# Kernel optimization log

Hardware: AMD Instinct MI355X
Metric: run time of the kernel (lower is better)

The kernel has to match this reference:

```python
import jax, jax.numpy as jnp
import numpy as np

N_GRAPHS = 100
BN_EPS = 1e-5
L = 4


def batch_norm(x, gamma, beta):
    # torch BatchNorm1d in training mode: biased batch statistics over the node dim
    mu = jnp.mean(x, axis=0)
    var = jnp.var(x, axis=0)
    return gamma * (x - mu) * jax.lax.rsqrt(var + BN_EPS) + beta


def setup_inputs() -> dict:
    key = jax.random.key(0)
    ks = jax.random.split(key, 24)
    N, E, IN, H, C = 50000, 600000, 128, 128, 10
    s = 0.05
    inp = {
        "h": jax.random.normal(ks[0], (N, IN), jnp.float32),
        "snorm_n": jax.random.uniform(ks[1], (N, 1), jnp.float32),
        "edge_src": jax.random.randint(ks[2], (E,), 0, N, jnp.int32),
        "edge_dst": jax.random.randint(ks[3], (E,), 0, N, jnp.int32),
        "graph_ids": jnp.sort(jax.random.randint(ks[4], (N,), 0, N_GRAPHS, jnp.int32)),
        # embedding_h
        "emb_W": jax.random.normal(ks[5], (IN, H), jnp.float32) * s,
        "emb_b": jnp.zeros((H,), jnp.float32),
        # per-layer GIN params, stacked over L layers
        "eps": jnp.zeros((L,), jnp.float32),
        "W1": jax.random.normal(ks[6], (L, H, H), jnp.float32) * s,
        "b1": jnp.zeros((L, H), jnp.float32),
        "g1": jnp.ones((L, H), jnp.float32),   # MLP internal BN gamma
        "be1": jnp.zeros((L, H), jnp.float32),  # MLP internal BN beta
        "W2": jax.random.normal(ks[7], (L, H, H), jnp.float32) * s,
        "b2": jnp.zeros((L, H), jnp.float32),
        "ga": jnp.ones((L, H), jnp.float32),    # ApplyNodeFunc BN gamma
        "ba": jnp.zeros((L, H), jnp.float32),
        "gl": jnp.ones((L, H), jnp.float32),    # GINLayer node BN gamma
        "bl": jnp.zeros((L, H), jnp.float32),
        # linears_prediction (L+1 of them)
        "pred_W": jax.random.normal(ks[8], (L + 1, H, C), jnp.float32) * s,
        "pred_b": jnp.zeros((L + 1, C), jnp.float32),
    }
    return inp


def reference(h, snorm_n, edge_src, edge_dst, graph_ids, emb_W, emb_b, eps,
              W1, b1, g1, be1, W2, b2, ga, ba, gl, bl, pred_W, pred_b):
    N = h.shape[0]
    h = h @ emb_W + emb_b  # embedding_h
    hidden_rep = [h]
    for i in range(L):
        h_in = h
        # sum-aggregate neighbor features (irregular gather + scatter-add)
        neigh = jax.ops.segment_sum(h[edge_src], edge_dst, num_segments=N)
        z = (1.0 + eps[i]) * h + neigh
        # ApplyNodeFunc: MLP (lin->BN->relu->lin) then BN then relu
        z = jax.nn.relu(batch_norm(z @ W1[i] + b1[i], g1[i], be1[i]))
        z = z @ W2[i] + b2[i]
        z = jax.nn.relu(batch_norm(z, ga[i], ba[i]))
        z = z * snorm_n                      # graph_norm
        z = batch_norm(z, gl[i], bl[i])      # batch_norm
        z = jax.nn.relu(z)
        h = h_in + z                         # residual (dropout p=0)
        hidden_rep.append(h)
    score = jnp.zeros((N_GRAPHS, pred_W.shape[-1]), h.dtype)
    for i, hr in enumerate(hidden_rep):
        pooled = jax.ops.segment_sum(hr, graph_ids, num_segments=N_GRAPHS)
        score = score + pooled @ pred_W[i] + pred_b[i]
    return score
```

## Files before the change

### kernel.cpp

```cpp
#include <hip/hip_runtime.h>

#define HD __device__ __forceinline__

static constexpr int H = 128;
static constexpr int G = 100;
static constexpr int L = 4;
static constexpr int C = 10;
static constexpr int DEGCAP = 64;
static constexpr int CNT_PAD = 50048;

typedef __attribute__((ext_vector_type(8))) short short8;
typedef __attribute__((ext_vector_type(4))) float f32x4;

HD float bf2f(unsigned int u16) {
    return __uint_as_float(u16 << 16);
}
HD unsigned int f2bf(float f) {
    unsigned int u = __float_as_uint(f);
    u += 0x7fffu + ((u >> 16) & 1u);
    return u >> 16;
}

__global__ __launch_bounds__(256) void prep_kernel(
    const float* __restrict__ embW, const float* __restrict__ W1, const float* __restrict__ W2,
    unsigned short* __restrict__ WT, unsigned short* __restrict__ Hb,
    const int* __restrict__ src, const int* __restrict__ dst, int E,
    int* __restrict__ cnt, int* __restrict__ esrc) {
    int b = blockIdx.x;
    if (b < 576) {
        int mat = b >> 6;
        int bx = b & 63;
        if (b == 0 && threadIdx.x < 64)
            ((unsigned int*)Hb)[threadIdx.x] = 0u;
        const float* s = (mat == 0) ? embW
                       : (mat <= L) ? W1 + (size_t)(mat - 1) * H * H
                                    : W2 + (size_t)(mat - 1 - L) * H * H;
        int t = bx * 256 + threadIdx.x;
        int col = t >> 7, k = t & 127;
        WT[(size_t)mat * H * H + col * H + k] = (unsigned short)f2bf(s[(size_t)k * H + col]);
    } else {
        int e = (b - 576) * 256 + threadIdx.x;
        if (e < E) {
            int d = dst[e];
            int pos = atomicAdd(&cnt[d], 1) & (DEGCAP - 1);
            esrc[(size_t)d * DEGCAP + pos] = src[e] + 1;
        }
    }
}

__global__ __launch_bounds__(1024, 2) void aggemm_kernel(
    const unsigned short* __restrict__ HbZ, const int* __restrict__ cnt,
    const int* __restrict__ esrc, const float* __restrict__ eps, int layer,
    const unsigned short* __restrict__ WT, const float* __restrict__ bias,
    unsigned short* __restrict__ outB, int N,
    float* __restrict__ sum_out, float* __restrict__ sq_out,
    int* __restrict__ ctr, int ntiles) {
    __shared__ unsigned short As[64 * 136];
    __shared__ int epsh[64][16];
    __shared__ int degsh[64];
    __shared__ int tilesh;
    int tid = threadIdx.x;
    int w = tid >> 6, lane = tid & 63, q = lane >> 4, m = lane & 15;
    float e1 = 1.0f + eps[layer];

    int mrow = (w >> 2) * 16;
    int colbase = (w & 3) * 32;
    short8 bfrag[2][4];
#pragma unroll
    for (int nt = 0; nt < 2; ++nt) {
        const unsigned short* wc = WT + (size_t)(colbase + nt * 16 + m) * H;
#pragma unroll
        for (int kk = 0; kk < 4; ++kk)
            bfrag[nt][kk] = *(const short8*)&wc[kk * 32 + q * 8];
    }
    float bs2[2] = {bias[colbase + m], bias[colbase + 16 + m]};

    for (;;) {
        if (tid == 0) tilesh = atomicAdd(ctr, 1);
        __syncthreads();
        int tile = tilesh;
        if (tile >= ntiles) break;
        int row0 = tile * 64;

        {
            int n = tid >> 4, u = tid & 15;
            int nd = min(row0 + n, N - 1);
            epsh[n][u] = esrc[(size_t)nd * DEGCAP + u];
            if (tid < 64) {
                int nn = row0 + tid;
                degsh[tid] = (nn < N) ? min(cnt[nn], DEGCAP) : 0;
            }
        }
        __syncthreads();

        {
            const unsigned int* H2 = (const unsigned int*)HbZ;
#pragma unroll
            for (int i = 0; i < 4; ++i) {
                int r = w * 4 + i;
                int node = row0 + r;
                unsigned int out = 0;
                if (node < N) {
                    unsigned int hv = H2[(size_t)(node + 1) * 64 + lane];
                    float ax = e1 * bf2f(hv & 0xffffu);
                    float ay = e1 * bf2f(hv >> 16);
                    int deg = degsh[r];
                    if (deg > 0) {
                        unsigned int v[16];
#pragma unroll
                        for (int u = 0; u < 16; ++u) v[u] = H2[(size_t)epsh[r][u] * 64 + lane];
                        float sx[4] = {0.f, 0.f, 0.f, 0.f}, sy[4] = {0.f, 0.f, 0.f, 0.f};
#pragma unroll
                        for (int u = 0; u < 16; ++u) {
                            sx[u & 3] += bf2f(v[u] & 0xffffu);
                            sy[u & 3] += bf2f(v[u] >> 16);
                        }
                        ax += (sx[0] + sx[1]) + (sx[2] + sx[3]);
                        ay += (sy[0] + sy[1]) + (sy[2] + sy[3]);
                        if (deg > 16) {
                            const int* ep = esrc + (size_t)node * DEGCAP;
                            int degPad = min((deg + 15) & ~15, DEGCAP);
                            for (int j = 16; j < degPad; j += 16) {
                                unsigned int vv[16];
#pragma unroll
                                for (int u = 0; u < 16; ++u) vv[u] = H2[(size_t)ep[j + u] * 64 + lane];
                                float tx[4] = {0.f, 0.f, 0.f, 0.f}, ty[4] = {0.f, 0.f, 0.f, 0.f};
#pragma unroll
                                for (int u = 0; u < 16; ++u) {
                                    tx[u & 3] += bf2f(vv[u] & 0xffffu);
                                    ty[u & 3] += bf2f(vv[u] >> 16);
                                }
                                ax += (tx[0] + tx[1]) + (tx[2] + tx[3]);
                                ay += (ty[0] + ty[1]) + (ty[2] + ty[3]);
                            }
                        }
                    }
                    out = f2bf(ax) | (f2bf(ay) << 16);
                }
                *(unsigned int*)&As[r * 136 + lane * 2] = out;
            }
        }
        __syncthreads();

        f32x4 acc[2] = {(f32x4){0.f, 0.f, 0.f, 0.f}, (f32x4){0.f, 0.f, 0.f, 0.f}};
#pragma unroll
        for (int kk = 0; kk < 4; ++kk) {
            short8 af = *(const short8*)&As[(mrow + m) * 136 + kk * 32 + q * 8];
#pragma unroll
            for (int nt = 0; nt < 2; ++nt)
                acc[nt] = __builtin_amdgcn_mfma_f32_16x16x32_bf16(af, bfrag[nt][kk], acc[nt], 0, 0, 0);
        }

        float s[2] = {0.f, 0.f}, qq[2] = {0.f, 0.f};
#pragma unroll
        for (int nt = 0; nt < 2; ++nt) {
            int gcol = colbase + nt * 16 + m;
#pragma unroll
            for (int rg = 0; rg < 4; ++rg) {
                int grow = row0 + mrow + q * 4 + rg;
                float v = acc[nt][rg] + bs2[nt];
                if (grow < N) {
                    outB[(size_t)grow * H + gcol] = (unsigned short)f2bf(v);
                    s[nt] += v;
                    qq[nt] += v * v;
                }
            }
        }
#pragma unroll
        for (int nt = 0; nt < 2; ++nt) {
            s[nt] += __shfl_xor(s[nt], 16); s[nt] += __shfl_xor(s[nt], 32);
            qq[nt] += __shfl_xor(qq[nt], 16); qq[nt] += __shfl_xor(qq[nt], 32);
        }
        __syncthreads();
        float* SS = (float*)As;
        float* QQ = SS + 4 * H;
        if (q == 0) {
#pragma unroll
            for (int nt = 0; nt < 2; ++nt) {
                int col = colbase + nt * 16 + m;
                SS[(w >> 2) * H + col] = s[nt];
                QQ[(w >> 2) * H + col] = qq[nt];
            }
        }
        __syncthreads();
        if (tid < H) {
            atomicAdd(&sum_out[tid], SS[tid] + SS[H + tid] + SS[2 * H + tid] + SS[3 * H + tid]);
            atomicAdd(&sq_out[tid], QQ[tid] + QQ[H + tid] + QQ[2 * H + tid] + QQ[3 * H + tid]);
        }
    }
}

template <bool ABF16, bool TRANS, bool STATS, bool POOLF, bool HOFF>
__global__ __launch_bounds__(256, 4) void mgemm_kernel(
    const float* __restrict__ Af, const unsigned short* __restrict__ Ab,
    const unsigned short* __restrict__ WT, const float* __restrict__ bias,
    const float* __restrict__ sum_in, const float* __restrict__ sq_in,
    const float* __restrict__ gam, const float* __restrict__ bet, float invN,
    unsigned short* __restrict__ outB,
    int N, float* __restrict__ sum_out, float* __restrict__ sq_out,
    const int* __restrict__ gids, float* __restrict__ pool) {
    __shared__ unsigned short As[64 * 136];
    __shared__ float cas[H], ccs[H];
    int tid = threadIdx.x;
    int w = tid >> 6, lane = tid & 63, q = lane >> 4, m = lane & 15;
    int row0 = blockIdx.x * 64;
    int colbase = w * 32;

    short8 bfrag[2][4];
#pragma unroll
    for (int nt = 0; nt < 2; ++nt) {
        const unsigned short* wc = WT + (size_t)(colbase + nt * 16 + m) * H;
#pragma unroll
        for (int kk = 0; kk < 4; ++kk)
            bfrag[nt][kk] = *(const short8*)&wc[kk * 32 + q * 8];
    }

    if (TRANS) {
        if (tid < H) {
            float mu = sum_in[tid] * invN;
            float var = sq_in[tid] * invN - mu * mu;
            float inv = rsqrtf(var + 1e-5f);
            float a = gam[tid] * inv;
            cas[tid] = a;
            ccs[tid] = bet[tid] - mu * a;
        }
        __syncthreads();
    }

    {
        int cc = tid & 15, rg = tid >> 4;
        int c0 = cc * 8;
        float a8[8], b8[8];
        if (TRANS) {
#pragma unroll
            for (int j = 0; j < 8; ++j) { a8[j] = cas[c0 + j]; b8[j] = ccs[c0 + j]; }
        }
#pragma unroll
        for (int rr = 0; rr < 4; ++rr) {
            int r = rg * 4 + rr;
            int gr = row0 + r;
            uint4 o = {0u, 0u, 0u, 0u};
            if (ABF16 && !TRANS) {
                if (gr < N) o = *(const uint4*)&Ab[(size_t)gr * H + c0];
            } else {
                float v[8] = {0.f, 0.f, 0.f, 0.f, 0.f, 0.f, 0.f, 0.f};
                if (gr < N) {
                    if (ABF16) {
                        uint4 x = *(const uint4*)&Ab[(size_t)gr * H + c0];
                        v[0] = bf2f(x.x & 0xffffu); v[1] = bf2f(x.x >> 16);
                        v[2] = bf2f(x.y & 0xffffu); v[3] = bf2f(x.y >> 16);
                        v[4] = bf2f(x.z & 0xffffu); v[5] = bf2f(x.z >> 16);
                        v[6] = bf2f(x.w & 0xffffu); v[7] = bf2f(x.w >> 16);
                    } else {
                        float4 x0 = *(const float4*)&Af[(size_t)gr * H + c0];
                        float4 x1 = *(const float4*)&Af[(size_t)gr * H + c0 + 4];
                        v[0] = x0.x; v[1] = x0.y; v[2] = x0.z; v[3] = x0.w;
                        v[4] = x1.x; v[5] = x1.y; v[6] = x1.z; v[7] = x1.w;
                    }
                }
                if (TRANS) {
#pragma unroll
                    for (int j = 0; j < 8; ++j) v[j] = fmaxf(a8[j] * v[j] + b8[j], 0.f);
                }
                o.x = f2bf(v[0]) | (f2bf(v[1]) << 16);
                o.y = f2bf(v[2]) | (f2bf(v[3]) << 16);
                o.z = f2bf(v[4]) | (f2bf(v[5]) << 16);
                o.w = f2bf(v[6]) | (f2bf(v[7]) << 16);
            }
            *(uint4*)&As[r * 136 + c0] = o;
        }
    }
    __syncthreads();

    f32x4 acc[4][2];
#pragma unroll
    for (int mt = 0; mt < 4; ++mt)
#pragma unroll
        for (int nt = 0; nt < 2; ++nt) acc[mt][nt] = (f32x4){0.f, 0.f, 0.f, 0.f};
#pragma unroll
    for (int kk = 0; kk < 4; ++kk) {
        short8 af[4];
#pragma unroll
        for (int mt = 0; mt < 4; ++mt)
            af[mt] = *(const short8*)&As[(mt * 16 + m) * 136 + kk * 32 + q * 8];
#pragma unroll
        for (int mt = 0; mt < 4; ++mt)
#pragma unroll
            for (int nt = 0; nt < 2; ++nt)
                acc[mt][nt] = __builtin_amdgcn_mfma_f32_16x16x32_bf16(
                    af[mt], bfrag[nt][kk], acc[mt][nt], 0, 0, 0);
    }

    float bs2[2] = {bias[colbase + m], bias[colbase + 16 + m]};
    float s[2] = {0.f, 0.f}, qq[2] = {0.f, 0.f};
#pragma unroll
    for (int mt = 0; mt < 4; ++mt)
#pragma unroll
        for (int nt = 0; nt < 2; ++nt) {
            int gcol = colbase + nt * 16 + m;
#pragma unroll
            for (int rg = 0; rg < 4; ++rg) {
                int grow = row0 + mt * 16 + q * 4 + rg;
                float v = acc[mt][nt][rg] + bs2[nt];
                if (grow < N) {
                    outB[(size_t)(HOFF ? grow + 1 : grow) * H + gcol] = (unsigned short)f2bf(v);
                    if (STATS) {
                        s[nt] += v;
                        qq[nt] += v * v;
                    }
                }
            }
        }

    if (STATS) {
#pragma unroll
        for (int nt = 0; nt < 2; ++nt) {
            float sv = s[nt], qv = qq[nt];
            sv += __shfl_xor(sv, 16); sv += __shfl_xor(sv, 32);
            qv += __shfl_xor(qv, 16); qv += __shfl_xor(qv, 32);
            if (q == 0) {
                atomicAdd(&sum_out[colbase + nt * 16 + m], sv);
                atomicAdd(&sq_out[colbase + nt * 16 + m], qv);
            }
        }
    }

    if (POOLF) {
        int g0 = gids[row0];
        int gL = gids[min(row0 + 63, N - 1)];
        float s0[2] = {0.f, 0.f}, s1[2] = {0.f, 0.f};
#pragma unroll
        for (int mt = 0; mt < 4; ++mt)
#pragma unroll
            for (int rg = 0; rg < 4; ++rg) {
                int grow = row0 + mt * 16 + q * 4 + rg;
                if (grow < N) {
                    int g = gids[grow];
#pragma unroll
                    for (int nt = 0; nt < 2; ++nt) {
                        float v = acc[mt][nt][rg] + bs2[nt];
                        if (g == g0) s0[nt] += v;
                        else if (g == gL) s1[nt] += v;
                        else atomicAdd(&pool[g * H + colbase + nt * 16 + m], v);
                    }
                }
            }
#pragma unroll
        for (int nt = 0; nt < 2; ++nt) {
            int col = colbase + nt * 16 + m;
            float sv = s0[nt];
            sv += __shfl_xor(sv, 16); sv += __shfl_xor(sv, 32);
            if (q == 0) atomicAdd(&pool[g0 * H + col], sv);
            if (gL != g0) {
                float tv = s1[nt];
                tv += __shfl_xor(tv, 16); tv += __shfl_xor(tv, 32);
                if (q == 0) atomicAdd(&pool[gL * H + col], tv);
            }
        }
    }
}

__global__ __launch_bounds__(256) void statsv_kernel(const unsigned short* __restrict__ UB,
                                                     const float* __restrict__ snorm,
                                                     const float* __restrict__ sum2, const float* __restrict__ sq2,
                                                     const float* __restrict__ ga, const float* __restrict__ ba,
                                                     float invN, int N,
                                                     float* __restrict__ sum3, float* __restrict__ sq3) {
    __shared__ float cas[H], ccs[H];
    int t = threadIdx.x;
    if (t < H) {
        float m = sum2[t] * invN;
        float var = sq2[t] * invN - m * m;
        float inv = rsqrtf(var + 1e-5f);
        float a = ga[t] * inv;
        cas[t] = a;
        ccs[t] = ba[t] - m * a;
    }
    __syncthreads();
    int col2 = t & 63, part = t >> 6;
    int c0 = col2 * 2, c1 = c0 + 1;
    float a0 = cas[c0], b0 = ccs[c0], a1 = cas[c1], b1 = ccs[c1];
    float s0 = 0.f, q0 = 0.f, s1 = 0.f, q1 = 0.f;
    const unsigned int* U2 = (const unsigned int*)UB;
    for (int r0 = blockIdx.x * 16 + part * 4; r0 < N; r0 += gridDim.x * 16) {
        unsigned int vv[4];
        float sn4[4];
#pragma unroll
        for (int k = 0; k < 4; ++k) {
            int r = r0 + k;
            bool ok = r < N;
            sn4[k] = ok ? snorm[r] : 0.f;
            vv[k] = ok ? U2[(size_t)r * 64 + col2] : 0u;
        }
#pragma unroll
        for (int k = 0; k < 4; ++k) {
            float v0 = fmaxf(a0 * bf2f(vv[k] & 0xffffu) + b0, 0.f) * sn4[k];
            float v1 = fmaxf(a1 * bf2f(vv[k] >> 16) + b1, 0.f) * sn4[k];
            s0 += v0; q0 += v0 * v0;
            s1 += v1; q1 += v1 * v1;
        }
    }
    __shared__ float S[4][H], Q[4][H];
    S[part][c0] = s0; S[part][c1] = s1;
    Q[part][c0] = q0; Q[part][c1] = q1;
    __syncthreads();
    if (t < H) {
        atomicAdd(&sum3[t], S[0][t] + S[1][t] + S[2][t] + S[3][t]);
        atomicAdd(&sq3[t], Q[0][t] + Q[1][t] + Q[2][t] + Q[3][t]);
    }
}

__global__ __launch_bounds__(256) void tail_kernel(unsigned short* __restrict__ HbZ,
                                                   const unsigned short* __restrict__ UB,
                                                   const float* __restrict__ snorm,
                                                   const float* __restrict__ sum2, const float* __restrict__ sq2,
                                                   const float* __restrict__ ga, const float* __restrict__ ba,
                                                   const float* __restrict__ sum3, const float* __restrict__ sq3,
                                                   const float* __restrict__ gl, const float* __restrict__ bl,
                                                   float invN, const int* __restrict__ gids,
                                                   float* __restrict__ pool, int N) {
    __shared__ float ca2[H], cc2[H], ca3[H], cc3[H];
    __shared__ float PS[16][H];
    int t = threadIdx.x;
    if (t < H) {
        float m2 = sum2[t] * invN, v2 = sq2[t] * invN - m2 * m2;
        float i2 = rsqrtf(v2 + 1e-5f), a2 = ga[t] * i2;
        ca2[t] = a2; cc2[t] = ba[t] - m2 * a2;
        float m3 = sum3[t] * invN, v3 = sq3[t] * invN - m3 * m3;
        float i3 = rsqrtf(v3 + 1e-5f), a3 = gl[t] * i3;
        ca3[t] = a3; cc3[t] = bl[t] - m3 * a3;
    }
    __syncthreads();
    int row0 = blockIdx.x * 32;
    int colg = t & 15, rowg = t >> 4;
    int c0 = colg * 8;
    float A2[8], B2[8], A3[8], B3[8];
#pragma unroll
    for (int j = 0; j < 8; ++j) {
        A2[j] = ca2[c0 + j]; B2[j] = cc2[c0 + j];
        A3[j] = ca3[c0 + j]; B3[j] = cc3[c0 + j];
    }
    int g0 = gids[row0];
    int gL = gids[min(row0 + 31, N - 1)];
    float p0[8] = {0.f, 0.f, 0.f, 0.f, 0.f, 0.f, 0.f, 0.f};
    float p1[8] = {0.f, 0.f, 0.f, 0.f, 0.f, 0.f, 0.f, 0.f};

    uint4 uv[2], hv[2];
    float sn2[2];
    int gg[2];
#pragma unroll
    for (int rr = 0; rr < 2; ++rr) {
        int grow = row0 + rowg * 2 + rr;
        bool ok = grow < N;
        sn2[rr] = ok ? snorm[grow] : 0.f;
        gg[rr] = ok ? gids[grow] : g0;
        uv[rr] = ok ? *(const uint4*)&UB[(size_t)grow * H + c0] : (uint4){0u, 0u, 0u, 0u};
        hv[rr] = ok ? *(const uint4*)&HbZ[(size_t)(grow + 1) * H + c0] : (uint4){0u, 0u, 0u, 0u};
    }
#pragma unroll
    for (int rr = 0; rr < 2; ++rr) {
        int grow = row0 + rowg * 2 + rr;
        if (grow < N) {
            float u[8] = {bf2f(uv[rr].x & 0xffffu), bf2f(uv[rr].x >> 16),
                          bf2f(uv[rr].y & 0xffffu), bf2f(uv[rr].y >> 16),
                          bf2f(uv[rr].z & 0xffffu), bf2f(uv[rr].z >> 16),
                          bf2f(uv[rr].w & 0xffffu), bf2f(uv[rr].w >> 16)};
            float h[8] = {bf2f(hv[rr].x & 0xffffu), bf2f(hv[rr].x >> 16),
                          bf2f(hv[rr].y & 0xffffu), bf2f(hv[rr].y >> 16),
                          bf2f(hv[rr].z & 0xffffu), bf2f(hv[rr].z >> 16),
                          bf2f(hv[rr].w & 0xffffu), bf2f(hv[rr].w >> 16)};
#pragma unroll
            for (int j = 0; j < 8; ++j) {
                float v = fmaxf(A2[j] * u[j] + B2[j], 0.f) * sn2[rr];
                h[j] += fmaxf(A3[j] * v + B3[j], 0.f);
            }
            uint4 hb;
            hb.x = f2bf(h[0]) | (f2bf(h[1]) << 16);
            hb.y = f2bf(h[2]) | (f2bf(h[3]) << 16);
            hb.z = f2bf(h[4]) | (f2bf(h[5]) << 16);
            hb.w = f2bf(h[6]) | (f2bf(h[7]) << 16);
            *(uint4*)&HbZ[(size_t)(grow + 1) * H + c0] = hb;
            int g = gg[rr];
            if (g == g0) {
#pragma unroll
                for (int j = 0; j < 8; ++j) p0[j] += h[j];
            } else if (g == gL) {
#pragma unroll
                for (int j = 0; j < 8; ++j) p1[j] += h[j];
            } else {
#pragma unroll
                for (int j = 0; j < 8; ++j) atomicAdd(&pool[g * H + c0 + j], h[j]);
            }
        }
    }
#pragma unroll
    for (int j = 0; j < 8; ++j) PS[rowg][c0 + j] = p0[j];
    __syncthreads();
    if (t < H) {
        float s = 0.f;
#pragma unroll
        for (int g = 0; g < 16; ++g) s += PS[g][t];
        atomicAdd(&pool[g0 * H + t], s);
    }
    if (gL != g0) {
        __syncthreads();
#pragma unroll
        for (int j = 0; j < 8; ++j) PS[rowg][c0 + j] = p1[j];
        __syncthreads();
        if (t < H) {
            float s = 0.f;
#pragma unroll
            for (int g = 0; g < 16; ++g) s += PS[g][t];
            atomicAdd(&pool[gL * H + t], s);
        }
    }
}

__global__ __launch_bounds__(128) void final_kernel(const float* __restrict__ pool,
                                                    const float* __restrict__ pw,
                                                    const float* __restrict__ pb,
                                                    float* __restrict__ out) {
    int g = blockIdx.x, t = threadIdx.x;
    float acc[C];
#pragma unroll
    for (int c = 0; c < C; ++c) acc[c] = 0.f;
#pragma unroll
    for (int i = 0; i <= L; ++i) {
        float p = pool[(size_t)(i * G + g) * H + t];
        const float* wrow = pw + (size_t)(i * H + t) * C;
#pragma unroll
        for (int c = 0; c < C; ++c) acc[c] += p * wrow[c];
    }
#pragma unroll
    for (int c = 0; c < C; ++c) {
        float v = acc[c];
        v += __shfl_xor(v, 1);  v += __shfl_xor(v, 2);  v += __shfl_xor(v, 4);
        v += __shfl_xor(v, 8);  v += __shfl_xor(v, 16); v += __shfl_xor(v, 32);
        acc[c] = v;
    }
    __shared__ float Ws[2][C];
    if ((t & 63) == 0) {
        int wv = t >> 6;
#pragma unroll
        for (int c = 0; c < C; ++c) Ws[wv][c] = acc[c];
    }
    __syncthreads();
    if (t < C) {
        float s = Ws[0][t] + Ws[1][t];
#pragma unroll
        for (int i = 0; i <= L; ++i) s += pb[i * C + t];
        out[g * C + t] = s;
    }
}

extern "C" void kernel_launch(void* const* d_in, const int* in_sizes, int n_in,
                              void* d_out, int out_size, void* d_ws, size_t ws_size,
                              hipStream_t stream) {
    const float* h_in  = (const float*)d_in[0];
    const float* snorm = (const float*)d_in[1];
    const int* esrc_in = (const int*)d_in[2];
    const int* edst_in = (const int*)d_in[3];
    const int* gids    = (const int*)d_in[4];
    const float* embW = (const float*)d_in[5];
    const float* embB = (const float*)d_in[6];
    const float* eps  = (const float*)d_in[7];
    const float* W1   = (const float*)d_in[8];
    const float* b1   = (const float*)d_in[9];
    const float* g1   = (const float*)d_in[10];
    const float* be1  = (const float*)d_in[11];
    const float* W2   = (const float*)d_in[12];
    const float* b2   = (const float*)d_in[13];
    const float* ga   = (const float*)d_in[14];
    const float* ba   = (const float*)d_in[15];
    const float* gl   = (const float*)d_in[16];
    const float* bl   = (const float*)d_in[17];
    const float* predW = (const float*)d_in[18];
    const float* predB = (const float*)d_in[19];

    const int N = in_sizes[0] / H;
    const int E = in_sizes[2];
    const float invN = 1.0f / (float)N;

    float* ws = (float*)d_ws;
    float* POOL = ws;
    float* STATS = POOL + (size_t)(L + 1) * G * H;
    int* CTR = (int*)(STATS + (size_t)L * 6 * H);
    int* CNT = CTR + 64;
    int* ESRC = CNT + CNT_PAD;
    unsigned short* WT = (unsigned short*)(ESRC + (size_t)N * DEGCAP);
    unsigned short* Hb = WT + (size_t)9 * H * H;
    unsigned short* ZB = Hb + (size_t)(N + 1) * H;
    unsigned short* TB = ZB + (size_t)N * H;
    unsigned short* UB = ZB;

    size_t zbytes = ((size_t)(L + 1) * G * H + (size_t)L * 6 * H + 64 + CNT_PAD + (size_t)N * DEGCAP) * 4;
    hipMemsetAsync(POOL, 0, zbytes, stream);

    int prep_blocks = 576 + (E + 255) / 256;
    prep_kernel<<<prep_blocks, 256, 0, stream>>>(embW, W1, W2, WT, Hb,
                                                 esrc_in, edst_in, E, CNT, ESRC);

    int gblocks = (N + 63) / 64;
    mgemm_kernel<false, false, false, true, true><<<gblocks, 256, 0, stream>>>(
        h_in, nullptr, WT, embB, nullptr, nullptr, nullptr, nullptr, invN,
        Hb, N, nullptr, nullptr, gids, POOL);

    for (int i = 0; i < L; ++i) {
        float* S1 = STATS + (size_t)i * 6 * H;
        float* Q1 = S1 + H;
        float* S2 = Q1 + H;
        float* Q2 = S2 + H;
        float* S3 = Q2 + H;
        float* Q3 = S3 + H;
        aggemm_kernel<<<512, 1024, 0, stream>>>(
            Hb, CNT, ESRC, eps, i, WT + (size_t)(1 + i) * H * H, b1 + (size_t)i * H,
            TB, N, S1, Q1, CTR + i, gblocks);
        mgemm_kernel<true, true, true, false, false><<<gblocks, 256, 0, stream>>>(
            nullptr, TB, WT + (size_t)(1 + L + i) * H * H, b2 + (size_t)i * H,
            S1, Q1, g1 + (size_t)i * H, be1 + (size_t)i * H, invN,
            UB, N, S2, Q2, nullptr, nullptr);
        statsv_kernel<<<1024, 256, 0, stream>>>(UB, snorm, S2, Q2,
                                                ga + (size_t)i * H, ba + (size_t)i * H, invN, N, S3, Q3);
        tail_kernel<<<(N + 31) / 32, 256, 0, stream>>>(Hb, UB, snorm,
                                                       S2, Q2, ga + (size_t)i * H, ba + (size_t)i * H,
                                                       S3, Q3, gl + (size_t)i * H, bl + (size_t)i * H,
                                                       invN, gids, POOL + (size_t)(i + 1) * G * H, N);
    }
    final_kernel<<<G, 128, 0, stream>>>(POOL, predW, predB, (float*)d_out);
}
```

Measured before the change: 608.4 us.

## Fuse second GEMM, BN stats and tail into one grid-barrier layer kernel

New measurement: 1.031 ms. +69.4%, slower.

```diff
diff --git a/kernel.cpp b/kernel.cpp
--- a/kernel.cpp
+++ b/kernel.cpp
@@ -19,6 +19,25 @@
     unsigned int u = __float_as_uint(f);
     u += 0x7fffu + ((u >> 16) & 1u);
     return u >> 16;
+}
+
+HD float aload(const float* p) {
+    return __hip_atomic_load(p, __ATOMIC_RELAXED, __HIP_MEMORY_SCOPE_AGENT);
+}
+
+HD void gridbar(int* arr, int* rel, int nblk, int tid) {
+    __syncthreads();
+    if (tid == 0) {
+        __threadfence();
+        int t = __hip_atomic_fetch_add(arr, 1, __ATOMIC_ACQ_REL, __HIP_MEMORY_SCOPE_AGENT);
+        if (t == nblk - 1) {
+            __hip_atomic_store(rel, 1, __ATOMIC_RELEASE, __HIP_MEMORY_SCOPE_AGENT);
+        } else {
+            while (__hip_atomic_load(rel, __ATOMIC_ACQUIRE, __HIP_MEMORY_SCOPE_AGENT) == 0)
+                __builtin_amdgcn_s_sleep(2);
+        }
+    }
+    __syncthreads();
 }
 
 __global__ __launch_bounds__(256) void prep_kernel(
@@ -190,17 +209,11 @@
     }
 }
 
-template <bool ABF16, bool TRANS, bool STATS, bool POOLF, bool HOFF>
-__global__ __launch_bounds__(256, 4) void mgemm_kernel(
-    const float* __restrict__ Af, const unsigned short* __restrict__ Ab,
-    const unsigned short* __restrict__ WT, const float* __restrict__ bias,
-    const float* __restrict__ sum_in, const float* __restrict__ sq_in,
-    const float* __restrict__ gam, const float* __restrict__ bet, float invN,
-    unsigned short* __restrict__ outB,
-    int N, float* __restrict__ sum_out, float* __restrict__ sq_out,
-    const int* __restrict__ gids, float* __restrict__ pool) {
+__global__ __launch_bounds__(256, 4) void embed_kernel(
+    const float* __restrict__ Af, const unsigned short* __restrict__ WT,
+    const float* __restrict__ bias, unsigned short* __restrict__ outB,
+    int N, const int* __restrict__ gids, float* __restrict__ pool) {
     __shared__ unsigned short As[64 * 136];
-    __shared__ float cas[H], ccs[H];
     int tid = threadIdx.x;
     int w = tid >> 6, lane = tid & 63, q = lane >> 4, m = lane & 15;
     int row0 = blockIdx.x * 64;
@@ -215,53 +228,149 @@
             bfrag[nt][kk] = *(const short8*)&wc[kk * 32 + q * 8];
     }
 
-    if (TRANS) {
-        if (tid < H) {
-            float mu = sum_in[tid] * invN;
-            float var = sq_in[tid] * invN - mu * mu;
-            float inv = rsqrtf(var + 1e-5f);
-            float a = gam[tid] * inv;
-            cas[tid] = a;
-            ccs[tid] = bet[tid] - mu * a;
-        }
-        __syncthreads();
-    }
-
     {
         int cc = tid & 15, rg = tid >> 4;
         int c0 = cc * 8;
-        float a8[8], b8[8];
-        if (TRANS) {
-#pragma unroll
-            for (int j = 0; j < 8; ++j) { a8[j] = cas[c0 + j]; b8[j] = ccs[c0 + j]; }
-        }
 #pragma unroll
         for (int rr = 0; rr < 4; ++rr) {
             int r = rg * 4 + rr;
             int gr = row0 + r;
             uint4 o = {0u, 0u, 0u, 0u};
-            if (ABF16 && !TRANS) {
-                if (gr < N) o = *(const uint4*)&Ab[(size_t)gr * H + c0];
-            } else {
-                float v[8] = {0.f, 0.f, 0.f, 0.f, 0.f, 0.f, 0.f, 0.f};
-                if (gr < N) {
-                    if (ABF16) {
-                        uint4 x = *(const uint4*)&Ab[(size_t)gr * H + c0];
-                        v[0] = bf2f(x.x & 0xffffu); v[1] = bf2f(x.x >> 16);
-                        v[2] = bf2f(x.y & 0xffffu); v[3] = bf2f(x.y >> 16);
-                        v[4] = bf2f(x.z & 0xffffu); v[5] = bf2f(x.z >> 16);
-                        v[6] = bf2f(x.w & 0xffffu); v[7] = bf2f(x.w >> 16);
-                    } else {
-                        float4 x0 = *(const float4*)&Af[(size_t)gr * H + c0];
-                        float4 x1 = *(const float4*)&Af[(size_t)gr * H + c0 + 4];
-                        v[0] = x0.x; v[1] = x0.y; v[2] = x0.z; v[3] = x0.w;
-                        v[4] = x1.x; v[5] = x1.y; v[6] = x1.z; v[7] = x1.w;
-                    }
+            if (gr < N) {
+                float4 x0 = *(const float4*)&Af[(size_t)gr * H + c0];
+                float4 x1 = *(const float4*)&Af[(size_t)gr * H + c0 + 4];
+                o.x = f2bf(x0.x) | (f2bf(x0.y) << 16);
+                o.y = f2bf(x0.z) | (f2bf(x0.w) << 16);
+                o.z = f2bf(x1.x) | (f2bf(x1.y) << 16);
+                o.w = f2bf(x1.z) | (f2bf(x1.w) << 16);
+            }
+            *(uint4*)&As[r * 136 + c0] = o;
+        }
+    }
+    __syncthreads();
+
+    f32x4 acc[4][2];
+#pragma unroll
+    for (int mt = 0; mt < 4; ++mt)
+#pragma unroll
+        for (int nt = 0; nt < 2; ++nt) acc[mt][nt] = (f32x4){0.f, 0.f, 0.f, 0.f};
+#pragma unroll
+    for (int kk = 0; kk < 4; ++kk) {
+        short8 af[4];
+#pragma unroll
+        for (int mt = 0; mt < 4; ++mt)
+            af[mt] = *(const short8*)&As[(mt * 16 + m) * 136 + kk * 32 + q * 8];
+#pragma unroll
+        for (int mt = 0; mt < 4; ++mt)
+#pragma unroll
+            for (int nt = 0; nt < 2; ++nt)
+                acc[mt][nt] = __builtin_amdgcn_mfma_f32_16x16x32_bf16(
+                    af[mt], bfrag[nt][kk], acc[mt][nt], 0, 0, 0);
+    }
+
+    float bs2[2] = {bias[colbase + m], bias[colbase + 16 + m]};
+#pragma unroll
+    for (int mt = 0; mt < 4; ++mt)
+#pragma unroll
+        for (int nt = 0; nt < 2; ++nt) {
+            int gcol = colbase + nt * 16 + m;
+#pragma unroll
+            for (int rg = 0; rg < 4; ++rg) {
+                int grow = row0 + mt * 16 + q * 4 + rg;
+                float v = acc[mt][nt][rg] + bs2[nt];
+                if (grow < N) outB[(size_t)(grow + 1) * H + gcol] = (unsigned short)f2bf(v);
+            }
+        }
+
+    int g0 = gids[row0];
+    int gL = gids[min(row0 + 63, N - 1)];
+    float s0[2] = {0.f, 0.f}, s1[2] = {0.f, 0.f};
+#pragma unroll
+    for (int mt = 0; mt < 4; ++mt)
+#pragma unroll
+        for (int rg = 0; rg < 4; ++rg) {
+            int grow = row0 + mt * 16 + q * 4 + rg;
+            if (grow < N) {
+                int g = gids[grow];
+#pragma unroll
+                for (int nt = 0; nt < 2; ++nt) {
+                    float v = acc[mt][nt][rg] + bs2[nt];
+                    if (g == g0) s0[nt] += v;
+                    else if (g == gL) s1[nt] += v;
+                    else atomicAdd(&pool[g * H + colbase + nt * 16 + m], v);
                 }
-                if (TRANS) {
-#pragma unroll
-                    for (int j = 0; j < 8; ++j) v[j] = fmaxf(a8[j] * v[j] + b8[j], 0.f);
-                }
+            }
+        }
+#pragma unroll
+    for (int nt = 0; nt < 2; ++nt) {
+        int col = colbase + nt * 16 + m;
+        float sv = s0[nt];
+        sv += __shfl_xor(sv, 16); sv += __shfl_xor(sv, 32);
+        if (q == 0) atomicAdd(&pool[g0 * H + col], sv);
+        if (gL != g0) {
+            float tv = s1[nt];
+            tv += __shfl_xor(tv, 16); tv += __shfl_xor(tv, 32);
+            if (q == 0) atomicAdd(&pool[gL * H + col], tv);
+        }
+    }
+}
+
+__global__ __launch_bounds__(256, 4) void layer_kernel(
+    const unsigned short* __restrict__ TB, const unsigned short* __restrict__ WT2,
+    const float* __restrict__ b2v,
+    const float* __restrict__ S1, const float* __restrict__ Q1,
+    const float* __restrict__ g1v, const float* __restrict__ be1v,
+    const float* __restrict__ snorm,
+    float* __restrict__ S2, float* __restrict__ Q2,
+    float* __restrict__ S3, float* __restrict__ Q3,
+    const float* __restrict__ gav, const float* __restrict__ bav,
+    const float* __restrict__ glv, const float* __restrict__ blv,
+    unsigned short* __restrict__ Hb, const int* __restrict__ gids,
+    float* __restrict__ pool, float invN, int N, int* __restrict__ bar) {
+    __shared__ unsigned short As[64 * 136];
+    __shared__ float ca[H], cc[H];
+    __shared__ float sn[64];
+    __shared__ float PS[16][H];
+    int tid = threadIdx.x;
+    int w = tid >> 6, lane = tid & 63, q = lane >> 4, m = lane & 15;
+    int row0 = blockIdx.x * 64;
+    int colbase = w * 32;
+    int nblk = gridDim.x;
+
+    short8 bfrag[2][4];
+#pragma unroll
+    for (int nt = 0; nt < 2; ++nt) {
+        const unsigned short* wc = WT2 + (size_t)(colbase + nt * 16 + m) * H;
+#pragma unroll
+        for (int kk = 0; kk < 4; ++kk)
+            bfrag[nt][kk] = *(const short8*)&wc[kk * 32 + q * 8];
+    }
+    if (tid < H) {
+        float mu = S1[tid] * invN;
+        float var = Q1[tid] * invN - mu * mu;
+        float a = g1v[tid] * rsqrtf(var + 1e-5f);
+        ca[tid] = a;
+        cc[tid] = be1v[tid] - mu * a;
+    }
+    if (tid < 64) sn[tid] = (row0 + tid < N) ? snorm[row0 + tid] : 0.f;
+    __syncthreads();
+    {
+        int ccol = tid & 15, rg = tid >> 4;
+        int c0 = ccol * 8;
+        float a8[8], b8[8];
+#pragma unroll
+        for (int j = 0; j < 8; ++j) { a8[j] = ca[c0 + j]; b8[j] = cc[c0 + j]; }
+#pragma unroll
+        for (int rr = 0; rr < 4; ++rr) {
+            int r = rg * 4 + rr;
+            int gr = row0 + r;
+            uint4 o = {0u, 0u, 0u, 0u};
+            if (gr < N) {
+                uint4 x = *(const uint4*)&TB[(size_t)gr * H + c0];
+                float v[8] = {bf2f(x.x & 0xffffu), bf2f(x.x >> 16), bf2f(x.y & 0xffffu), bf2f(x.y >> 16),
+                              bf2f(x.z & 0xffffu), bf2f(x.z >> 16), bf2f(x.w & 0xffffu), bf2f(x.w >> 16)};
+#pragma unroll
+                for (int j = 0; j < 8; ++j) v[j] = fmaxf(a8[j] * v[j] + b8[j], 0.f);
                 o.x = f2bf(v[0]) | (f2bf(v[1]) << 16);
                 o.y = f2bf(v[2]) | (f2bf(v[3]) << 16);
                 o.z = f2bf(v[4]) | (f2bf(v[5]) << 16);
@@ -290,228 +399,151 @@
                 acc[mt][nt] = __builtin_amdgcn_mfma_f32_16x16x32_bf16(
                     af[mt], bfrag[nt][kk], acc[mt][nt], 0, 0, 0);
     }
-
-    float bs2[2] = {bias[colbase + m], bias[colbase + 16 + m]};
-    float s[2] = {0.f, 0.f}, qq[2] = {0.f, 0.f};
-#pragma unroll
-    for (int mt = 0; mt < 4; ++mt)
-#pragma unroll
-        for (int nt = 0; nt < 2; ++nt) {
-            int gcol = colbase + nt * 16 + m;
-#pragma unroll
-            for (int rg = 0; rg < 4; ++rg) {
-                int grow = row0 + mt * 16 + q * 4 + rg;
-                float v = acc[mt][nt][rg] + bs2[nt];
-                if (grow < N) {
-                    outB[(size_t)(HOFF ? grow + 1 : grow) * H + gcol] = (unsigned short)f2bf(v);
-                    if (STATS) {
-                        s[nt] += v;
-                        qq[nt] += v * v;
-                    }
+    {
+        float bs2[2] = {b2v[colbase + m], b2v[colbase + 16 + m]};
+        float s[2] = {0.f, 0.f}, qq[2] = {0.f, 0.f};
+#pragma unroll
+        for (int mt = 0; mt < 4; ++mt)
+#pragma unroll
+            for (int nt = 0; nt < 2; ++nt)
+#pragma unroll
+                for (int rg = 0; rg < 4; ++rg) {
+                    float v = acc[mt][nt][rg] + bs2[nt];
+                    acc[mt][nt][rg] = v;
+                    int grow = row0 + mt * 16 + q * 4 + rg;
+                    if (grow < N) { s[nt] += v; qq[nt] += v * v; }
                 }
-            }
-        }
-
-    if (STATS) {
 #pragma unroll
         for (int nt = 0; nt < 2; ++nt) {
             float sv = s[nt], qv = qq[nt];
             sv += __shfl_xor(sv, 16); sv += __shfl_xor(sv, 32);
             qv += __shfl_xor(qv, 16); qv += __shfl_xor(qv, 32);
             if (q == 0) {
-                atomicAdd(&sum_out[colbase + nt * 16 + m], sv);
-                atomicAdd(&sq_out[colbase + nt * 16 + m], qv);
-            }
-        }
-    }
-
-    if (POOLF) {
+                atomicAdd(&S2[colbase + nt * 16 + m], sv);
+                atomicAdd(&Q2[colbase + nt * 16 + m], qv);
+            }
+        }
+    }
+    gridbar(&bar[0], &bar[1], nblk, tid);
+
+    if (tid < H) {
+        float mu = aload(&S2[tid]) * invN;
+        float var = aload(&Q2[tid]) * invN - mu * mu;
+        float a = gav[tid] * rsqrtf(var + 1e-5f);
+        ca[tid] = a;
+        cc[tid] = bav[tid] - mu * a;
+    }
+    __syncthreads();
+    {
+        float s[2] = {0.f, 0.f}, qq[2] = {0.f, 0.f};
+#pragma unroll
+        for (int nt = 0; nt < 2; ++nt) {
+            int col = colbase + nt * 16 + m;
+            float a = ca[col], c = cc[col];
+#pragma unroll
+            for (int mt = 0; mt < 4; ++mt)
+#pragma unroll
+                for (int rg = 0; rg < 4; ++rg) {
+                    int r = mt * 16 + q * 4 + rg;
+                    float v = fmaxf(a * acc[mt][nt][rg] + c, 0.f) * sn[r];
+                    As[r * 136 + col] = (unsigned short)f2bf(v);
+                    if (row0 + r < N) { s[nt] += v; qq[nt] += v * v; }
+                }
+        }
+#pragma unroll
+        for (int nt = 0; nt < 2; ++nt) {
+            float sv = s[nt], qv = qq[nt];
+            sv += __shfl_xor(sv, 16); sv += __shfl_xor(sv, 32);
+            qv += __shfl_xor(qv, 16); qv += __shfl_xor(qv, 32);
+            if (q == 0) {
+                atomicAdd(&S3[colbase + nt * 16 + m], sv);
+                atomicAdd(&Q3[colbase + nt * 16 + m], qv);
+            }
+        }
+    }
+    gridbar(&bar[2], &bar[3], nblk, tid);
+
+    if (tid < H) {
+        float mu = aload(&S3[tid]) * invN;
+        float var = aload(&Q3[tid]) * invN - mu * mu;
+        float a = glv[tid] * rsqrtf(var + 1e-5f);
+        ca[tid] = a;
+        cc[tid] = blv[tid] - mu * a;
+    }
+    __syncthreads();
+    {
+        int colg = tid & 15, rowg = tid >> 4;
+        int c0 = colg * 8;
+        float A3[8], B3[8];
+#pragma unroll
+        for (int j = 0; j < 8; ++j) { A3[j] = ca[c0 + j]; B3[j] = cc[c0 + j]; }
         int g0 = gids[row0];
         int gL = gids[min(row0 + 63, N - 1)];
-        float s0[2] = {0.f, 0.f}, s1[2] = {0.f, 0.f};
-#pragma unroll
-        for (int mt = 0; mt < 4; ++mt)
-#pragma unroll
-            for (int rg = 0; rg < 4; ++rg) {
-                int grow = row0 + mt * 16 + q * 4 + rg;
-                if (grow < N) {
-                    int g = gids[grow];
-#pragma unroll
-                    for (int nt = 0; nt < 2; ++nt) {
-                        float v = acc[mt][nt][rg] + bs2[nt];
-                        if (g == g0) s0[nt] += v;
-                        else if (g == gL) s1[nt] += v;
-                        else atomicAdd(&pool[g * H + colbase + nt * 16 + m], v);
-                    }
+        float p0[8] = {0.f, 0.f, 0.f, 0.f, 0.f, 0.f, 0.f, 0.f};
+        float p1[8] = {0.f, 0.f, 0.f, 0.f, 0.f, 0.f, 0.f, 0.f};
+
+        uint4 hv[4];
+        int gg[4];
+#pragma unroll
+        for (int rr = 0; rr < 4; ++rr) {
+            int grow = row0 + rowg * 4 + rr;
+            bool ok = grow < N;
+            gg[rr] = ok ? gids[grow] : g0;
+            hv[rr] = ok ? *(const uint4*)&Hb[(size_t)(grow + 1) * H + c0] : (uint4){0u, 0u, 0u, 0u};
+        }
+#pragma unroll
+        for (int rr = 0; rr < 4; ++rr) {
+            int r = rowg * 4 + rr;
+            int grow = row0 + r;
+            if (grow < N) {
+                float h[8] = {bf2f(hv[rr].x & 0xffffu), bf2f(hv[rr].x >> 16),
+                              bf2f(hv[rr].y & 0xffffu), bf2f(hv[rr].y >> 16),
+                              bf2f(hv[rr].z & 0xffffu), bf2f(hv[rr].z >> 16),
+                              bf2f(hv[rr].w & 0xffffu), bf2f(hv[rr].w >> 16)};
+#pragma unroll
+                for (int j = 0; j < 8; ++j) {
+                    float v = bf2f(As[r * 136 + c0 + j]);
+                    h[j] += fmaxf(A3[j] * v + B3[j], 0.f);
                 }
-            }
-#pragma unroll
-        for (int nt = 0; nt < 2; ++nt) {
-            int col = colbase + nt * 16 + m;
-            float sv = s0[nt];
-            sv += __shfl_xor(sv, 16); sv += __shfl_xor(sv, 32);
-            if (q == 0) atomicAdd(&pool[g0 * H + col], sv);
-            if (gL != g0) {
-                float tv = s1[nt];
-                tv += __shfl_xor(tv, 16); tv += __shfl_xor(tv, 32);
-                if (q == 0) atomicAdd(&pool[gL * H + col], tv);
-            }
-        }
-    }
-}
-
-__global__ __launch_bounds__(256) void statsv_kernel(const unsigned short* __restrict__ UB,
-                                                     const float* __restrict__ snorm,
-                                                     const float* __restrict__ sum2, const float* __restrict__ sq2,
-                                                     const float* __restrict__ ga, const float* __restrict__ ba,
-                                                     float invN, int N,
-                                                     float* __restrict__ sum3, float* __restrict__ sq3) {
-    __shared__ float cas[H], ccs[H];
-    int t = threadIdx.x;
-    if (t < H) {
-        float m = sum2[t] * invN;
-        float var = sq2[t] * invN - m * m;
-        float inv = rsqrtf(var + 1e-5f);
-        float a = ga[t] * inv;
-        cas[t] = a;
-        ccs[t] = ba[t] - m * a;
-    }
-    __syncthreads();
-    int col2 = t & 63, part = t >> 6;
-    int c0 = col2 * 2, c1 = c0 + 1;
-    float a0 = cas[c0], b0 = ccs[c0], a1 = cas[c1], b1 = ccs[c1];
-    float s0 = 0.f, q0 = 0.f, s1 = 0.f, q1 = 0.f;
-    const unsigned int* U2 = (const unsigned int*)UB;
-    for (int r0 = blockIdx.x * 16 + part * 4; r0 < N; r0 += gridDim.x * 16) {
-        unsigned int vv[4];
-        float sn4[4];
-#pragma unroll
-        for (int k = 0; k < 4; ++k) {
-            int r = r0 + k;
-            bool ok = r < N;
-            sn4[k] = ok ? snorm[r] : 0.f;
-            vv[k] = ok ? U2[(size_t)r * 64 + col2] : 0u;
-        }
-#pragma unroll
-        for (int k = 0; k < 4; ++k) {
-            float v0 = fmaxf(a0 * bf2f(vv[k] & 0xffffu) + b0, 0.f) * sn4[k];
-            float v1 = fmaxf(a1 * bf2f(vv[k] >> 16) + b1, 0.f) * sn4[k];
-            s0 += v0; q0 += v0 * v0;
-            s1 += v1; q1 += v1 * v1;
-        }
-    }
-    __shared__ float S[4][H], Q[4][H];
-    S[part][c0] = s0; S[part][c1] = s1;
-    Q[part][c0] = q0; Q[part][c1] = q1;
-    __syncthreads();
-    if (t < H) {
-        atomicAdd(&sum3[t], S[0][t] + S[1][t] + S[2][t] + S[3][t]);
-        atomicAdd(&sq3[t], Q[0][t] + Q[1][t] + Q[2][t] + Q[3][t]);
-    }
-}
-
-__global__ __launch_bounds__(256) void tail_kernel(unsigned short* __restrict__ HbZ,
-                                                   const unsigned short* __restrict__ UB,
-                                                   const float* __restrict__ snorm,
-                                                   const float* __restrict__ sum2, const float* __restrict__ sq2,
-                                                   const float* __restrict__ ga, const float* __restrict__ ba,
-                                                   const float* __restrict__ sum3, const float* __restrict__ sq3,
-                                                   const float* __restrict__ gl, const float* __restrict__ bl,
-                                                   float invN, const int* __restrict__ gids,
-                                                   float* __restrict__ pool, int N) {
-    __shared__ float ca2[H], cc2[H], ca3[H], cc3[H];
-    __shared__ float PS[16][H];
-    int t = threadIdx.x;
-    if (t < H) {
-        float m2 = sum2[t] * invN, v2 = sq2[t] * invN - m2 * m2;
-        float i2 = rsqrtf(v2 + 1e-5f), a2 = ga[t] * i2;
-        ca2[t] = a2; cc2[t] = ba[t] - m2 * a2;
-        float m3 = sum3[t] * invN, v3 = sq3[t] * invN - m3 * m3;
-        float i3 = rsqrtf(v3 + 1e-5f), a3 = gl[t] * i3;
-        ca3[t] = a3; cc3[t] = bl[t] - m3 * a3;
-    }
-    __syncthreads();
-    int row0 = blockIdx.x * 32;
-    int colg = t & 15, rowg = t >> 4;
-    int c0 = colg * 8;
-    float A2[8], B2[8], A3[8], B3[8];
-#pragma unroll
-    for (int j = 0; j < 8; ++j) {
-        A2[j] = ca2[c0 + j]; B2[j] = cc2[c0 + j];
-        A3[j] = ca3[c0 + j]; B3[j] = cc3[c0 + j];
-    }
-    int g0 = gids[row0];
-    int gL = gids[min(row0 + 31, N - 1)];
-    float p0[8] = {0.f, 0.f, 0.f, 0.f, 0.f, 0.f, 0.f, 0.f};
-    float p1[8] = {0.f, 0.f, 0.f, 0.f, 0.f, 0.f, 0.f, 0.f};
-
-    uint4 uv[2], hv[2];
-    float sn2[2];
-    int gg[2];
-#pragma unroll
-    for (int rr = 0; rr < 2; ++rr) {
-        int grow = row0 + rowg * 2 + rr;
-        bool ok = grow < N;
-        sn2[rr] = ok ? snorm[grow] : 0.f;
-        gg[rr] = ok ? gids[grow] : g0;
-        uv[rr] = ok ? *(const uint4*)&UB[(size_t)grow * H + c0] : (uint4){0u, 0u, 0u, 0u};
-        hv[rr] = ok ? *(const uint4*)&HbZ[(size_t)(grow + 1) * H + c0] : (uint4){0u, 0u, 0u, 0u};
-    }
-#pragma unroll
-    for (int rr = 0; rr < 2; ++rr) {
-        int grow = row0 + rowg * 2 + rr;
-        if (grow < N) {
-            float u[8] = {bf2f(uv[rr].x & 0xffffu), bf2f(uv[rr].x >> 16),
-                          bf2f(uv[rr].y & 0xffffu), bf2f(uv[rr].y >> 16),
-                          bf2f(uv[rr].z & 0xffffu), bf2f(uv[rr].z >> 16),
-                          bf2f(uv[rr].w & 0xffffu), bf2f(uv[rr].w >> 16)};
-            float h[8] = {bf2f(hv[rr].x & 0xffffu), bf2f(hv[rr].x >> 16),
-                          bf2f(hv[rr].y & 0xffffu), bf2f(hv[rr].y >> 16),
-                          bf2f(hv[rr].z & 0xffffu), bf2f(hv[rr].z >> 16),
-                          bf2f(hv[rr].w & 0xffffu), bf2f(hv[rr].w >> 16)};
-#pragma unroll
-            for (int j = 0; j < 8; ++j) {
-                float v = fmaxf(A2[j] * u[j] + B2[j], 0.f) * sn2[rr];
-                h[j] += fmaxf(A3[j] * v + B3[j], 0.f);
-            }
-            uint4 hb;
-            hb.x = f2bf(h[0]) | (f2bf(h[1]) << 16);
-            hb.y = f2bf(h[2]) | (f2bf(h[3]) << 16);
-            hb.z = f2bf(h[4]) | (f2bf(h[5]) << 16);
-            hb.w = f2bf(h[6]) | (f2bf(h[7]) << 16);
-            *(uint4*)&HbZ[(size_t)(grow + 1) * H + c0] = hb;
-            int g = gg[rr];
-            if (g == g0) {
-#pragma unroll
-                for (int j = 0; j < 8; ++j) p0[j] += h[j];
-            } else if (g == gL) {
-#pragma unroll
-                for (int j = 0; j < 8; ++j) p1[j] += h[j];
-            } else {
-#pragma unroll
-                for (int j = 0; j < 8; ++j) atomicAdd(&pool[g * H + c0 + j], h[j]);
-            }
-        }
-    }
-#pragma unroll
-    for (int j = 0; j < 8; ++j) PS[rowg][c0 + j] = p0[j];
-    __syncthreads();
-    if (t < H) {
-        float s = 0.f;
-#pragma unroll
-        for (int g = 0; g < 16; ++g) s += PS[g][t];
-        atomicAdd(&pool[g0 * H + t], s);
-    }
-    if (gL != g0) {
+                uint4 hb;
+                hb.x = f2bf(h[0]) | (f2bf(h[1]) << 16);
+                hb.y = f2bf(h[2]) | (f2bf(h[3]) << 16);
+                hb.z = f2bf(h[4]) | (f2bf(h[5]) << 16);
+                hb.w = f2bf(h[6]) | (f2bf(h[7]) << 16);
+                *(uint4*)&Hb[(size_t)(grow + 1) * H + c0] = hb;
+                int g = gg[rr];
+                if (g == g0) {
+#pragma unroll
+                    for (int j = 0; j < 8; ++j) p0[j] += h[j];
+                } else if (g == gL) {
+#pragma unroll
+                    for (int j = 0; j < 8; ++j) p1[j] += h[j];
+                } else {
+#pragma unroll
+                    for (int j = 0; j < 8; ++j) atomicAdd(&pool[g * H + c0 + j], h[j]);
+                }
+            }
+        }
+#pragma unroll
+        for (int j = 0; j < 8; ++j) PS[rowg][c0 + j] = p0[j];
         __syncthreads();
-#pragma unroll
-        for (int j = 0; j < 8; ++j) PS[rowg][c0 + j] = p1[j];
-        __syncthreads();
-        if (t < H) {
+        if (tid < H) {
             float s = 0.f;
 #pragma unroll
-            for (int g = 0; g < 16; ++g) s += PS[g][t];
-            atomicAdd(&pool[gL * H + t], s);
+            for (int g = 0; g < 16; ++g) s += PS[g][tid];
+            atomicAdd(&pool[g0 * H + tid], s);
+        }
+        if (gL != g0) {
+            __syncthreads();
+#pragma unroll
+            for (int j = 0; j < 8; ++j) PS[rowg][c0 + j] = p1[j];
+            __syncthreads();
+            if (tid < H) {
+                float s = 0.f;
+#pragma unroll
+                for (int g = 0; g < 16; ++g) s += PS[g][tid];
+                atomicAdd(&pool[gL * H + tid], s);
+            }
         }
     }
 }
@@ -584,14 +616,12 @@
     float* ws = (float*)d_ws;
     float* POOL = ws;
     float* STATS = POOL + (size_t)(L + 1) * G * H;
-    int* CTR = (int*)(STATS + (size_t)L * 6 * H);
-    int* CNT = CTR + 64;
+    int* CTRBAR = (int*)(STATS + (size_t)L * 6 * H);
+    int* CNT = CTRBAR + 64;
     int* ESRC = CNT + CNT_PAD;
     unsigned short* WT = (unsigned short*)(ESRC + (size_t)N * DEGCAP);
     unsigned short* Hb = WT + (size_t)9 * H * H;
-    unsigned short* ZB = Hb + (size_t)(N + 1) * H;
-    unsigned short* TB = ZB + (size_t)N * H;
-    unsigned short* UB = ZB;
+    unsigned short* TB = Hb + (size_t)(N + 1) * H;
 
     size_t zbytes = ((size_t)(L + 1) * G * H + (size_t)L * 6 * H + 64 + CNT_PAD + (size_t)N * DEGCAP) * 4;
     hipMemsetAsync(POOL, 0, zbytes, stream);
@@ -601,9 +631,7 @@
                                                  esrc_in, edst_in, E, CNT, ESRC);
 
     int gblocks = (N + 63) / 64;
-    mgemm_kernel<false, false, false, true, true><<<gblocks, 256, 0, stream>>>(
-        h_in, nullptr, WT, embB, nullptr, nullptr, nullptr, nullptr, invN,
-        Hb, N, nullptr, nullptr, gids, POOL);
+    embed_kernel<<<gblocks, 256, 0, stream>>>(h_in, WT, embB, Hb, N, gids, POOL);
 
     for (int i = 0; i < L; ++i) {
         float* S1 = STATS + (size_t)i * 6 * H;
@@ -614,17 +642,13 @@
         float* Q3 = S3 + H;
         aggemm_kernel<<<512, 1024, 0, stream>>>(
             Hb, CNT, ESRC, eps, i, WT + (size_t)(1 + i) * H * H, b1 + (size_t)i * H,
-            TB, N, S1, Q1, CTR + i, gblocks);
-        mgemm_kernel<true, true, true, false, false><<<gblocks, 256, 0, stream>>>(
-            nullptr, TB, WT + (size_t)(1 + L + i) * H * H, b2 + (size_t)i * H,
-            S1, Q1, g1 + (size_t)i * H, be1 + (size_t)i * H, invN,
-            UB, N, S2, Q2, nullptr, nullptr);
-        statsv_kernel<<<1024, 256, 0, stream>>>(UB, snorm, S2, Q2,
-                                                ga + (size_t)i * H, ba + (size_t)i * H, invN, N, S3, Q3);
-        tail_kernel<<<(N + 31) / 32, 256, 0, stream>>>(Hb, UB, snorm,
-                                                       S2, Q2, ga + (size_t)i * H, ba + (size_t)i * H,
-                                                       S3, Q3, gl + (size_t)i * H, bl + (size_t)i * H,
-                                                       invN, gids, POOL + (size_t)(i + 1) * G * H, N);
+            TB, N, S1, Q1, CTRBAR + i, gblocks);
+        layer_kernel<<<gblocks, 256, 0, stream>>>(
+            TB, WT + (size_t)(1 + L + i) * H * H, b2 + (size_t)i * H,
+            S1, Q1, g1 + (size_t)i * H, be1 + (size_t)i * H, snorm,
+            S2, Q2, S3, Q3,
+            ga + (size_t)i * H, ba + (size_t)i * H, gl + (size_t)i * H, bl + (size_t)i * H,
+            Hb, gids, POOL + (size_t)(i + 1) * G * H, invN, N, CTRBAR + 16 + i * 4);
     }
     final_kernel<<<G, 128, 0, stream>>>(POOL, predW, predB, (float*)d_out);
 }
```
